# Performance work log

Measured on AMD Instinct MI355X. Metric: run time of the kernel, lower is better.

Reference implementation:

```python
import jax, jax.numpy as jnp
import numpy as np

N_ATOMS = 100000
N_PAIRS = 2000000
N_EMB = 30
N_DIST = 100
N_HID = 60


def setup_inputs() -> dict:
    key = jax.random.key(0)
    ks = jax.random.split(key, 9)
    atom_features = jax.random.normal(ks[0], (N_ATOMS, N_EMB), dtype=jnp.float32)
    distance = jax.random.uniform(ks[1], (N_PAIRS, N_DIST), dtype=jnp.float32)
    # tf.segment_sum requires sorted segment ids
    distance_membership_i = jnp.sort(jax.random.randint(ks[2], (N_PAIRS,), 0, N_ATOMS))
    distance_membership_j = jax.random.randint(ks[3], (N_PAIRS,), 0, N_ATOMS)
    # glorot-uniform weights; biases small random (trainable, nonzero for a nontrivial reference)
    def glorot(k, fan_in, fan_out):
        lim = np.sqrt(6.0 / (fan_in + fan_out)).astype(np.float32)
        return jax.random.uniform(k, (fan_in, fan_out), minval=-lim, maxval=lim, dtype=jnp.float32)
    W_cf = glorot(ks[4], N_EMB, N_HID)
    W_df = glorot(ks[5], N_DIST, N_HID)
    W_fc = glorot(ks[6], N_HID, N_EMB)
    b_cf = 0.1 * jax.random.normal(ks[7], (N_HID,), dtype=jnp.float32)
    b_df = 0.1 * jax.random.normal(ks[8], (N_HID,), dtype=jnp.float32)
    return dict(atom_features=atom_features, distance=distance,
                distance_membership_i=distance_membership_i,
                distance_membership_j=distance_membership_j,
                W_cf=W_cf, W_df=W_df, W_fc=W_fc, b_cf=b_cf, b_df=b_df)


def reference(atom_features, distance, distance_membership_i, distance_membership_j,
              W_cf, W_df, W_fc, b_cf, b_df):
    n_atoms = atom_features.shape[0]
    # [E, H] and [N, H]
    distance_hidden = distance @ W_df + b_df
    atom_hidden = atom_features @ W_cf + b_cf
    # gather-fuse-matmul-activate over edges
    outputs = distance_hidden * atom_hidden[distance_membership_j]  # [E, H]
    outputs = jnp.tanh(outputs @ W_fc)                              # [E, F]
    # self-interaction correction term
    output_ii = jnp.tanh((b_df * atom_hidden) @ W_fc)               # [N, F]
    # scatter-reduce over destination atoms
    agg = jax.ops.segment_sum(outputs, distance_membership_i, num_segments=n_atoms)
    return agg - output_ii + atom_features
```

## Files before the change

### kernel.cpp

```cpp
#include <hip/hip_runtime.h>
#include <hip/hip_bf16.h>

#define N_ATOMS 100000
#define N_PAIRS 2000000
#define N_EMB 30
#define N_DIST 100
#define N_HID 60

#define TE 64
#define NTILES (N_PAIRS / TE)
#define EBLOCKS 768

typedef short bf16x8 __attribute__((ext_vector_type(8)));
typedef float f32x4 __attribute__((ext_vector_type(4)));

__device__ __forceinline__ ushort f2bf(float f) {
    __hip_bfloat16 h = __float2bfloat16(f);
    return __builtin_bit_cast(ushort, h);
}
__device__ __forceinline__ float bf2f(ushort u) {
    __hip_bfloat16 h = __builtin_bit_cast(__hip_bfloat16, u);
    return __bfloat162float(h);
}
__device__ __forceinline__ unsigned cvt_pk_bf16(float lo, float hi) {
    unsigned r;
    asm("v_cvt_pk_bf16_f32 %0, %1, %2" : "=v"(r) : "v"(lo), "v"(hi));
    return r;
}
__device__ __forceinline__ ushort f2bf_rne(float x) {
    return (ushort)cvt_pk_bf16(x, x);
}
__device__ __forceinline__ float fast_tanh(float x) {
    float e = __expf(2.0f * x);
    return 1.0f - 2.0f / (e + 1.0f);
}

__global__ __launch_bounds__(256) void atom_kernel(
    const float* __restrict__ af, const float* __restrict__ W_cf,
    const float* __restrict__ W_fc, const float* __restrict__ b_cf,
    const float* __restrict__ b_df, float* __restrict__ ah_out,
    float* __restrict__ out)
{
    __shared__ __align__(16) float ah_lds[4][N_HID];
    const int wave = threadIdx.x >> 6;
    const int lane = threadIdx.x & 63;
    const int n = blockIdx.x * 4 + wave;

    float ahv = 0.f;
    if (lane < N_HID) {
        ahv = b_cf[lane];
        #pragma unroll
        for (int k = 0; k < N_EMB; ++k)
            ahv = fmaf(af[(size_t)n * N_EMB + k], W_cf[k * N_HID + lane], ahv);
        ah_out[(size_t)n * N_HID + lane] = ahv;
        ah_lds[wave][lane] = ahv * b_df[lane];
    }
    __syncthreads();
    if (lane < N_EMB) {
        float s = 0.f;
        #pragma unroll
        for (int h = 0; h < N_HID; ++h)
            s = fmaf(ah_lds[wave][h], W_fc[h * N_EMB + lane], s);
        out[(size_t)n * N_EMB + lane] =
            af[(size_t)n * N_EMB + lane] - fast_tanh(s);
    }
}

__global__ __launch_bounds__(256, 3) void edge_kernel(
    const float* __restrict__ dist,
    const int* __restrict__ mi, const int* __restrict__ mj,
    const float* __restrict__ W_df, const float* __restrict__ W_fc,
    const float* __restrict__ b_df, const float* __restrict__ ah,
    float* out)
{
    __shared__ ushort A_lds[2][TE * 136];
    __shared__ ushort T_lds[TE * 72];
    __shared__ ushort S_lds[32 * 72];
    __shared__ int    mis[2][TE], mjs[2][TE];
    __shared__ int    seg_lds[TE];
    __shared__ int    seg_atom[TE];

    const int tid = threadIdx.x;
    const int wv = tid >> 6, lane = tid & 63;
    const int l4 = lane >> 4, ln = lane & 15;
    const int h1 = wv * 16 + ln;

    bf16x8 wdf[4];
    #pragma unroll
    for (int ks = 0; ks < 4; ++ks) {
        #pragma unroll
        for (int i = 0; i < 8; ++i) {
            int k = ks * 32 + l4 * 8 + i;
            float f = (k < N_DIST && h1 < N_HID) ? W_df[k * N_HID + h1] : 0.f;
            wdf[ks][i] = (short)f2bf(f);
        }
    }
    bf16x8 wfc[2][2];
    #pragma unroll
    for (int nf = 0; nf < 2; ++nf) {
        #pragma unroll
        for (int ks = 0; ks < 2; ++ks) {
            #pragma unroll
            for (int i = 0; i < 8; ++i) {
                int k = ks * 32 + l4 * 8 + i;
                int n = nf * 16 + ln;
                float f = (k < N_HID && n < N_EMB) ? W_fc[k * N_EMB + n] : 0.f;
                wfc[nf][ks][i] = (short)f2bf(f);
            }
        }
    }
    const float bdf1 = (h1 < N_HID) ? b_df[h1] : 0.f;

    int sdst[7];
    #pragma unroll
    for (int k = 0; k < 7; ++k) {
        int idx = k * 256 + tid;
        sdst[k] = (idx / 25) * 136 + (idx % 25) * 4;
    }

    for (int idx = tid; idx < 2 * TE * 36; idx += 256) {
        int b = idx / (TE * 36), rem = idx % (TE * 36);
        int r = rem / 36, c = 100 + rem % 36;
        A_lds[b][r * 136 + c] = 0;
    }

    const int t0 = (int)(((long long)blockIdx.x * NTILES) / EBLOCKS);
    const int t1 = (int)(((long long)(blockIdx.x + 1) * NTILES) / EBLOCKS);

    f32x4 pf[7];
    int pmi = 0, pmj = 0;

    auto stage_issue = [&](int t) {
        const f32x4* src = (const f32x4*)(dist + (size_t)t * TE * N_DIST);
        #pragma unroll
        for (int k = 0; k < 6; ++k)
            pf[k] = __builtin_nontemporal_load(&src[k * 256 + tid]);
        if (tid < 64) {
            pf[6] = __builtin_nontemporal_load(&src[6 * 256 + tid]);
            pmi = mi[t * TE + tid];
            pmj = mj[t * TE + tid];
        }
    };
    auto stage_write = [&](int buf) {
        #pragma unroll
        for (int k = 0; k < 7; ++k) {
            if (k < 6 || tid < 64) {
                f32x4 v = pf[k];
                uint2 w;
                w.x = cvt_pk_bf16(v[0], v[1]);
                w.y = cvt_pk_bf16(v[2], v[3]);
                *(uint2*)&A_lds[buf][sdst[k]] = w;
            }
        }
        if (tid < 64) { mis[buf][tid] = pmi; mjs[buf][tid] = pmj; }
    };

    stage_issue(t0);
    stage_write(0);
    __syncthreads();

    int cur = 0;
    for (int t = t0; t < t1; ++t) {
        const bool hasnext = (t + 1 < t1);

        float ahg[4][4];
        #pragma unroll
        for (int m = 0; m < 4; ++m) {
            #pragma unroll
            for (int r = 0; r < 4; ++r) {
                int el = 16 * m + l4 * 4 + r;
                int j = mjs[cur][el];
                ahg[m][r] = (h1 < N_HID) ? ah[(size_t)j * N_HID + h1] : 0.f;
            }
        }

        if (hasnext) stage_issue(t + 1);

        f32x4 acc1[4] = {{0,0,0,0},{0,0,0,0},{0,0,0,0},{0,0,0,0}};
        #pragma unroll
        for (int ks = 0; ks < 4; ++ks) {
            #pragma unroll
            for (int m = 0; m < 4; ++m) {
                bf16x8 a = *(const bf16x8*)&A_lds[cur][(16 * m + ln) * 136 + ks * 32 + l4 * 8];
                acc1[m] = __builtin_amdgcn_mfma_f32_16x16x32_bf16(a, wdf[ks], acc1[m], 0, 0, 0);
            }
        }

        #pragma unroll
        for (int m = 0; m < 4; ++m) {
            #pragma unroll
            for (int r = 0; r < 4; ++r) {
                int row = 16 * m + l4 * 4 + r;
                float tv = (acc1[m][r] + bdf1) * ahg[m][r];
                T_lds[row * 72 + h1] = f2bf_rne(tv);
            }
        }
        __syncthreads();

        f32x4 acc2[2] = {{0,0,0,0},{0,0,0,0}};
        #pragma unroll
        for (int ks = 0; ks < 2; ++ks) {
            bf16x8 a2 = *(const bf16x8*)&T_lds[(16 * wv + ln) * 72 + ks * 32 + l4 * 8];
            #pragma unroll
            for (int nf = 0; nf < 2; ++nf)
                acc2[nf] = __builtin_amdgcn_mfma_f32_16x16x32_bf16(a2, wfc[nf][ks], acc2[nf], 0, 0, 0);
        }
        #pragma unroll
        for (int nf = 0; nf < 2; ++nf) {
            uint2 w;
            w.x = cvt_pk_bf16(fast_tanh(acc2[nf][0]), fast_tanh(acc2[nf][1]));
            w.y = cvt_pk_bf16(fast_tanh(acc2[nf][2]), fast_tanh(acc2[nf][3]));
            *(uint2*)&S_lds[(nf * 16 + ln) * 72 + 16 * wv + l4 * 4] = w;
        }

        if (hasnext) stage_write(cur ^ 1);

        __syncthreads();

        int m_e = mis[cur][lane];
        int prevv = __shfl_up(m_e, 1);
        bool changed = (lane > 0) && (m_e != prevv);
        unsigned long long bmask = __ballot(changed);
        int segl = __popcll(bmask & ((2ull << lane) - 1ull));
        if (lane == 0 || changed) seg_atom[segl] = m_e;
        seg_lds[lane] = segl;
        int nseg = __popcll(bmask) + 1;

        int myseg = 16 * wv + ln;
        f32x4 acc3[2] = {{0,0,0,0},{0,0,0,0}};
        #pragma unroll
        for (int ks = 0; ks < 2; ++ks) {
            bf16x8 sfr;
            const int* sp = &seg_lds[ks * 32 + l4 * 8];
            #pragma unroll
            for (int i = 0; i < 8; ++i)
                sfr[i] = (sp[i] == myseg) ? (short)0x3F80 : (short)0;
            #pragma unroll
            for (int nf = 0; nf < 2; ++nf) {
                bf16x8 b = *(const bf16x8*)&S_lds[(nf * 16 + ln) * 72 + ks * 32 + l4 * 8];
                acc3[nf] = __builtin_amdgcn_mfma_f32_16x16x32_bf16(sfr, b, acc3[nf], 0, 0, 0);
            }
        }
        #pragma unroll
        for (int nf = 0; nf < 2; ++nf) {
            #pragma unroll
            for (int r = 0; r < 4; ++r) {
                int gs = 16 * wv + l4 * 4 + r;
                int f = nf * 16 + ln;
                if (gs < nseg && f < N_EMB) {
                    int atomId = seg_atom[gs];
                    atomicAdd(&out[(size_t)atomId * N_EMB + f], acc3[nf][r]);
                }
            }
        }
        cur ^= 1;
    }
}

extern "C" void kernel_launch(void* const* d_in, const int* in_sizes, int n_in,
                              void* d_out, int out_size, void* d_ws, size_t ws_size,
                              hipStream_t stream) {
    const float* af   = (const float*)d_in[0];
    const float* dist = (const float*)d_in[1];
    const int*   mi   = (const int*)d_in[2];
    const int*   mj   = (const int*)d_in[3];
    const float* W_cf = (const float*)d_in[4];
    const float* W_df = (const float*)d_in[5];
    const float* W_fc = (const float*)d_in[6];
    const float* b_cf = (const float*)d_in[7];
    const float* b_df = (const float*)d_in[8];
    float* out = (float*)d_out;
    float* ah  = (float*)d_ws;

    atom_kernel<<<N_ATOMS / 4, 256, 0, stream>>>(af, W_cf, W_fc, b_cf, b_df, ah, out);
    edge_kernel<<<EBLOCKS, 256, 0, stream>>>(dist, mi, mj, W_df, W_fc, b_df, ah, out);
}
```

Baseline: 303.1 us.

## Prefetch distance tiles two ahead with double register sets and lighter barriers

Deepens the global-load pipeline so each tile's distance data is fetched two iterations ahead, alternating between two register sets with a manually unrolled pair of tile bodies. W_fc fragments move from registers to LDS, the LDS row pitches shrink (136→104, 72→68), and __syncthreads is replaced by an explicit lgkmcnt wait plus s_barrier. The aim is to hide HBM latency for the streamed distance matrix without raising register pressure, at the cost of extra VGPRs for the second prefetch set and possible LDS bank conflicts from the new pitches. The K padding in A now only covers columns 100–103, yet the MFMA loop reads k up to 127, so it relies on zeroed W_df rows for those columns.

```diff
diff --git a/kernel.cpp b/kernel.cpp
--- a/kernel.cpp
+++ b/kernel.cpp
@@ -18,10 +18,6 @@
     __hip_bfloat16 h = __float2bfloat16(f);
     return __builtin_bit_cast(ushort, h);
 }
-__device__ __forceinline__ float bf2f(ushort u) {
-    __hip_bfloat16 h = __builtin_bit_cast(__hip_bfloat16, u);
-    return __bfloat162float(h);
-}
 __device__ __forceinline__ unsigned cvt_pk_bf16(float lo, float hi) {
     unsigned r;
     asm("v_cvt_pk_bf16_f32 %0, %1, %2" : "=v"(r) : "v"(lo), "v"(hi));
@@ -33,6 +29,11 @@
 __device__ __forceinline__ float fast_tanh(float x) {
     float e = __expf(2.0f * x);
     return 1.0f - 2.0f / (e + 1.0f);
+}
+__device__ __forceinline__ void lds_barrier() {
+    asm volatile("s_waitcnt lgkmcnt(0)" ::: "memory");
+    __builtin_amdgcn_s_barrier();
+    __builtin_amdgcn_sched_barrier(0);
 }
 
 __global__ __launch_bounds__(256) void atom_kernel(
@@ -73,9 +74,10 @@
     const float* __restrict__ b_df, const float* __restrict__ ah,
     float* out)
 {
-    __shared__ ushort A_lds[2][TE * 136];
-    __shared__ ushort T_lds[TE * 72];
-    __shared__ ushort S_lds[32 * 72];
+    __shared__ ushort A_lds[2][TE * 104];
+    __shared__ ushort T_lds[TE * 68];
+    __shared__ ushort S_lds[32 * 68];
+    __shared__ ushort WFC[4 * 64 * 8];
     __shared__ int    mis[2][TE], mjs[2][TE];
     __shared__ int    seg_lds[TE];
     __shared__ int    seg_atom[TE];
@@ -95,17 +97,20 @@
             wdf[ks][i] = (short)f2bf(f);
         }
     }
-    bf16x8 wfc[2][2];
-    #pragma unroll
-    for (int nf = 0; nf < 2; ++nf) {
-        #pragma unroll
-        for (int ks = 0; ks < 2; ++ks) {
-            #pragma unroll
-            for (int i = 0; i < 8; ++i) {
-                int k = ks * 32 + l4 * 8 + i;
-                int n = nf * 16 + ln;
-                float f = (k < N_HID && n < N_EMB) ? W_fc[k * N_EMB + n] : 0.f;
-                wfc[nf][ks][i] = (short)f2bf(f);
+    if (wv == 0) {
+        #pragma unroll
+        for (int nf = 0; nf < 2; ++nf) {
+            #pragma unroll
+            for (int ks = 0; ks < 2; ++ks) {
+                bf16x8 w;
+                #pragma unroll
+                for (int i = 0; i < 8; ++i) {
+                    int k = ks * 32 + l4 * 8 + i;
+                    int n = nf * 16 + ln;
+                    float f = (k < N_HID && n < N_EMB) ? W_fc[k * N_EMB + n] : 0.f;
+                    w[i] = (short)f2bf(f);
+                }
+                *(bf16x8*)&WFC[(nf * 2 + ks) * 512 + lane * 8] = w;
             }
         }
     }
@@ -115,37 +120,36 @@
     #pragma unroll
     for (int k = 0; k < 7; ++k) {
         int idx = k * 256 + tid;
-        sdst[k] = (idx / 25) * 136 + (idx % 25) * 4;
-    }
-
-    for (int idx = tid; idx < 2 * TE * 36; idx += 256) {
-        int b = idx / (TE * 36), rem = idx % (TE * 36);
-        int r = rem / 36, c = 100 + rem % 36;
-        A_lds[b][r * 136 + c] = 0;
-    }
+        sdst[k] = (idx / 25) * 104 + (idx % 25) * 4;
+    }
+    for (int idx = tid; idx < 2 * TE * 4; idx += 256) {
+        int b = idx / (TE * 4), rem = idx % (TE * 4);
+        A_lds[b][(rem >> 2) * 104 + 100 + (rem & 3)] = 0;
+    }
+    if (tid < 64) T_lds[tid] = 0;
 
     const int t0 = (int)(((long long)blockIdx.x * NTILES) / EBLOCKS);
     const int t1 = (int)(((long long)(blockIdx.x + 1) * NTILES) / EBLOCKS);
 
-    f32x4 pf[7];
-    int pmi = 0, pmj = 0;
-
-    auto stage_issue = [&](int t) {
+    f32x4 P0[7], P1[7];
+    int pmi0 = 0, pmj0 = 0, pmi1 = 0, pmj1 = 0;
+
+    auto issue = [&](int t, f32x4 (&P)[7], int& pmi, int& pmj) {
         const f32x4* src = (const f32x4*)(dist + (size_t)t * TE * N_DIST);
         #pragma unroll
         for (int k = 0; k < 6; ++k)
-            pf[k] = __builtin_nontemporal_load(&src[k * 256 + tid]);
+            P[k] = __builtin_nontemporal_load(&src[k * 256 + tid]);
         if (tid < 64) {
-            pf[6] = __builtin_nontemporal_load(&src[6 * 256 + tid]);
+            P[6] = __builtin_nontemporal_load(&src[6 * 256 + tid]);
             pmi = mi[t * TE + tid];
             pmj = mj[t * TE + tid];
         }
     };
-    auto stage_write = [&](int buf) {
+    auto writeA = [&](int buf, f32x4 (&P)[7], int pmi, int pmj) {
         #pragma unroll
         for (int k = 0; k < 7; ++k) {
             if (k < 6 || tid < 64) {
-                f32x4 v = pf[k];
+                f32x4 v = P[k];
                 uint2 w;
                 w.x = cvt_pk_bf16(v[0], v[1]);
                 w.y = cvt_pk_bf16(v[2], v[3]);
@@ -155,14 +159,15 @@
         if (tid < 64) { mis[buf][tid] = pmi; mjs[buf][tid] = pmj; }
     };
 
-    stage_issue(t0);
-    stage_write(0);
+    issue(t0, P0, pmi0, pmj0);
+    writeA(0, P0, pmi0, pmj0);
+    if (t0 + 1 < t1) issue(t0 + 1, P1, pmi1, pmj1);
     __syncthreads();
 
     int cur = 0;
-    for (int t = t0; t < t1; ++t) {
-        const bool hasnext = (t + 1 < t1);
-
+
+    auto tile_body = [&](int t, f32x4 (&Pi)[7], int& pmiI, int& pmjI,
+                         f32x4 (&Pw)[7], int& pmiW, int& pmjW) {
         float ahg[4][4];
         #pragma unroll
         for (int m = 0; m < 4; ++m) {
@@ -173,15 +178,14 @@
                 ahg[m][r] = (h1 < N_HID) ? ah[(size_t)j * N_HID + h1] : 0.f;
             }
         }
-
-        if (hasnext) stage_issue(t + 1);
+        if (t + 2 < t1) issue(t + 2, Pi, pmiI, pmjI);
 
         f32x4 acc1[4] = {{0,0,0,0},{0,0,0,0},{0,0,0,0},{0,0,0,0}};
         #pragma unroll
         for (int ks = 0; ks < 4; ++ks) {
             #pragma unroll
             for (int m = 0; m < 4; ++m) {
-                bf16x8 a = *(const bf16x8*)&A_lds[cur][(16 * m + ln) * 136 + ks * 32 + l4 * 8];
+                bf16x8 a = *(const bf16x8*)&A_lds[cur][(16 * m + ln) * 104 + ks * 32 + l4 * 8];
                 acc1[m] = __builtin_amdgcn_mfma_f32_16x16x32_bf16(a, wdf[ks], acc1[m], 0, 0, 0);
             }
         }
@@ -192,30 +196,32 @@
             for (int r = 0; r < 4; ++r) {
                 int row = 16 * m + l4 * 4 + r;
                 float tv = (acc1[m][r] + bdf1) * ahg[m][r];
-                T_lds[row * 72 + h1] = f2bf_rne(tv);
-            }
-        }
-        __syncthreads();
+                T_lds[row * 68 + h1] = f2bf_rne(tv);
+            }
+        }
+        lds_barrier();
 
         f32x4 acc2[2] = {{0,0,0,0},{0,0,0,0}};
         #pragma unroll
         for (int ks = 0; ks < 2; ++ks) {
-            bf16x8 a2 = *(const bf16x8*)&T_lds[(16 * wv + ln) * 72 + ks * 32 + l4 * 8];
-            #pragma unroll
-            for (int nf = 0; nf < 2; ++nf)
-                acc2[nf] = __builtin_amdgcn_mfma_f32_16x16x32_bf16(a2, wfc[nf][ks], acc2[nf], 0, 0, 0);
+            bf16x8 a2 = *(const bf16x8*)&T_lds[(16 * wv + ln) * 68 + ks * 32 + l4 * 8];
+            #pragma unroll
+            for (int nf = 0; nf < 2; ++nf) {
+                bf16x8 w = *(const bf16x8*)&WFC[(nf * 2 + ks) * 512 + lane * 8];
+                acc2[nf] = __builtin_amdgcn_mfma_f32_16x16x32_bf16(a2, w, acc2[nf], 0, 0, 0);
+            }
         }
         #pragma unroll
         for (int nf = 0; nf < 2; ++nf) {
             uint2 w;
             w.x = cvt_pk_bf16(fast_tanh(acc2[nf][0]), fast_tanh(acc2[nf][1]));
             w.y = cvt_pk_bf16(fast_tanh(acc2[nf][2]), fast_tanh(acc2[nf][3]));
-            *(uint2*)&S_lds[(nf * 16 + ln) * 72 + 16 * wv + l4 * 4] = w;
-        }
-
-        if (hasnext) stage_write(cur ^ 1);
-
-        __syncthreads();
+            *(uint2*)&S_lds[(nf * 16 + ln) * 68 + 16 * wv + l4 * 4] = w;
+        }
+
+        if (t + 1 < t1) writeA(cur ^ 1, Pw, pmiW, pmjW);
+
+        lds_barrier();
 
         int m_e = mis[cur][lane];
         int prevv = __shfl_up(m_e, 1);
@@ -237,7 +243,7 @@
                 sfr[i] = (sp[i] == myseg) ? (short)0x3F80 : (short)0;
             #pragma unroll
             for (int nf = 0; nf < 2; ++nf) {
-                bf16x8 b = *(const bf16x8*)&S_lds[(nf * 16 + ln) * 72 + ks * 32 + l4 * 8];
+                bf16x8 b = *(const bf16x8*)&S_lds[(nf * 16 + ln) * 68 + ks * 32 + l4 * 8];
                 acc3[nf] = __builtin_amdgcn_mfma_f32_16x16x32_bf16(sfr, b, acc3[nf], 0, 0, 0);
             }
         }
@@ -254,6 +260,13 @@
             }
         }
         cur ^= 1;
+    };
+
+    int t = t0;
+    while (t < t1) {
+        tile_body(t, P0, pmi0, pmj0, P1, pmi1, pmj1); ++t;
+        if (t >= t1) break;
+        tile_body(t, P1, pmi1, pmj1, P0, pmi0, pmj0); ++t;
     }
 }
 
```

After: 304.8 us. About the same (+0.6%).
